# Optimization experiments

Measured on AMD Instinct MI355X. Metric: run time of the kernel, lower is better.

The kernel has to match this reference:

```python
import jax, jax.numpy as jnp
import numpy as np

D_MODEL = 1024
NUM_HEADS = 16
THETA = 10000.0


def _rope(x, pos):
    # x: [B, H, S, d_k], pos: [B, S] int
    d = x.shape[-1]
    half = d // 2
    inv_freq = THETA ** (-(jnp.arange(half, dtype=jnp.float32) * 2.0) / d)  # [half]
    ang = pos.astype(jnp.float32)[..., None] * inv_freq                     # [B, S, half]
    cos = jnp.cos(ang)[:, None, :, :]  # [B, 1, S, half]
    sin = jnp.sin(ang)[:, None, :, :]
    x1 = x[..., 0::2]
    x2 = x[..., 1::2]
    r1 = x1 * cos - x2 * sin
    r2 = x1 * sin + x2 * cos
    return jnp.stack([r1, r2], axis=-1).reshape(x.shape)


def setup_inputs() -> dict:
    key = jax.random.key(0)
    ks = jax.random.split(key, 5)
    B, S, D = 2, 2048, D_MODEL
    scale = 1.0 / np.sqrt(D)
    x = jax.random.normal(ks[0], (B, S, D), dtype=jnp.float32)
    token_positions = jnp.broadcast_to(jnp.arange(S, dtype=jnp.int32), (B, S))
    Wq = jax.random.normal(ks[1], (D, D), dtype=jnp.float32) * scale
    Wk = jax.random.normal(ks[2], (D, D), dtype=jnp.float32) * scale
    Wv = jax.random.normal(ks[3], (D, D), dtype=jnp.float32) * scale
    Wo = jax.random.normal(ks[4], (D, D), dtype=jnp.float32) * scale
    return {"x": x, "token_positions": token_positions, "Wq": Wq, "Wk": Wk, "Wv": Wv, "Wo": Wo}


def reference(x, token_positions, Wq, Wk, Wv, Wo):
    B, S, D = x.shape
    H = NUM_HEADS
    dk = D // H
    # Linear: y = x @ W.T (torch nn.Linear convention, no bias)
    q = jnp.einsum('bsd,od->bso', x, Wq).reshape(B, S, H, dk).transpose(0, 2, 1, 3)
    k = jnp.einsum('bsd,od->bso', x, Wk).reshape(B, S, H, dk).transpose(0, 2, 1, 3)
    v = jnp.einsum('bsd,od->bso', x, Wv).reshape(B, S, H, dk).transpose(0, 2, 1, 3)
    q = _rope(q, token_positions)
    k = _rope(k, token_positions)
    scores = jnp.einsum('bhqd,bhkd->bhqk', q, k) / jnp.sqrt(jnp.float32(dk))
    causal = jnp.tril(jnp.ones((S, S), dtype=bool))
    scores = jnp.where(causal, scores, jnp.finfo(scores.dtype).min)
    attn = jax.nn.softmax(scores, axis=-1)
    out = jnp.einsum('bhqk,bhkd->bhqd', attn, v)  # [B, H, S, dk]
    out = out.transpose(0, 2, 1, 3).reshape(B, S, D)
    return jnp.einsum('bsd,od->bso', out, Wo)
```

## Files before the change

### kernel.cpp

```cpp
#include <hip/hip_runtime.h>
#include <stdint.h>

#define S_LEN 2048
#define DMODEL 1024
#define NHEAD 16
#define DK 64
#define BATCH 2

typedef __attribute__((ext_vector_type(8))) short bf16x8;
typedef __attribute__((ext_vector_type(4))) float f32x4;
typedef __attribute__((ext_vector_type(16))) float f32x16;
typedef __attribute__((ext_vector_type(2))) unsigned int uint2v;

__device__ __forceinline__ unsigned short f2bf(float f) {
  union { float f; unsigned u; } x; x.f = f;
  unsigned u = x.u;
  return (unsigned short)((u + 0x7fffu + ((u >> 16) & 1u)) >> 16);
}

__device__ __forceinline__ uint cvt_pk_bf16(float a, float b) {
  uint r;
  asm("v_cvt_pk_bf16_f32 %0, %1, %2" : "=v"(r) : "v"(a), "v"(b));
  return r;
}

__device__ __forceinline__ uint2v permswap(uint a, uint b) {
#if __has_builtin(__builtin_amdgcn_permlane32_swap)
  auto rr = __builtin_amdgcn_permlane32_swap(a, b, false, false);
  uint2v r; r.x = rr[0]; r.y = rr[1];
  return r;
#else
  uint ax = __shfl_xor(a, 32), bx = __shfl_xor(b, 32);
  int hi = (threadIdx.x & 63) >> 5;
  uint2v r; r.x = hi ? bx : a; r.y = hi ? b : ax;
  return r;
#endif
}

__device__ __forceinline__ void gload_lds16(const void* g, void* l) {
  __builtin_amdgcn_global_load_lds(
      (const __attribute__((address_space(1))) unsigned int*)g,
      (__attribute__((address_space(3))) unsigned int*)l, 16, 0, 0);
}

#define QSCALE 0.18033688011112042f

__global__ __launch_bounds__(256) void cast_inputs(
    const float4* __restrict__ x,
    const float4* __restrict__ wq, const float4* __restrict__ wk,
    const float4* __restrict__ wv, const float4* __restrict__ wo,
    ushort4* __restrict__ xb, ushort4* __restrict__ wqkvb, ushort4* __restrict__ wob,
    const int* __restrict__ pos, float2* __restrict__ rope)
{
  int i = blockIdx.x * 256 + threadIdx.x;
  const int NCAST = (1 << 21);
  if (i < NCAST) {
    float4 v; ushort4* dst;
    if (i < (1 << 20)) {
      v = x[i]; dst = xb + i;
    } else {
      int j = i - (1 << 20);
      int wsel = j >> 18;
      int o = j & ((1 << 18) - 1);
      const float4* src = (wsel == 0) ? wq : (wsel == 1) ? wk : (wsel == 2) ? wv : wo;
      v = src[o];
      dst = (wsel < 3) ? (wqkvb + ((size_t)wsel << 18) + o) : (wob + o);
    }
    ushort4 r;
    r.x = f2bf(v.x); r.y = f2bf(v.y); r.z = f2bf(v.z); r.w = f2bf(v.w);
    *dst = r;
  } else {
    int idx = i - NCAST;
    if (idx < 4096 * 32) {
      int ps = idx >> 5;
      int fi = idx & 31;
      float p = (float)pos[ps];
      float freq = exp2f(-(float)fi * 0.41524101186092096f);
      float ang = p * freq;
      rope[idx] = make_float2(cosf(ang), sinf(ang));
    }
  }
}

template<int EPI>
__global__ __launch_bounds__(256) void gemm_bt(
    const ushort* __restrict__ A, const ushort* __restrict__ Bw,
    const float2* __restrict__ rope,
    ushort* __restrict__ Qb, ushort* __restrict__ Kb, ushort* __restrict__ Vg,
    float* __restrict__ Out)
{
  constexpr int Kdim = 1024;
  __shared__ ushort At[128 * 64];
  __shared__ ushort Bt[128 * 64];
  const int bm = blockIdx.x & 31;
  const int bn = blockIdx.x >> 5;
  const int tid = threadIdx.x;
  const int w = tid >> 6, lane = tid & 63;
  const int wr = w >> 1, wc = w & 1;
  const int lrow = lane >> 3;
  const int lch = lane & 7;

  f32x4 acc[4][4];
#pragma unroll
  for (int i = 0; i < 4; ++i)
#pragma unroll
    for (int j = 0; j < 4; ++j) acc[i][j] = (f32x4){0.f, 0.f, 0.f, 0.f};

  const size_t abase = (size_t)(bm * 128) * Kdim;
  const size_t bbase = (size_t)(bn * 128) * Kdim;

  for (int kt = 0; kt < Kdim / 64; ++kt) {
#pragma unroll
    for (int inst = 0; inst < 4; ++inst) {
      int r = w * 32 + inst * 8 + lrow;
      int gc = lch ^ (r & 7);
      gload_lds16(A + abase + (size_t)r * Kdim + kt * 64 + gc * 8,
                  &At[(w * 32 + inst * 8) * 64]);
      gload_lds16(Bw + bbase + (size_t)r * Kdim + kt * 64 + gc * 8,
                  &Bt[(w * 32 + inst * 8) * 64]);
    }
    __syncthreads();
    __builtin_amdgcn_s_setprio(1);
#pragma unroll
    for (int kk = 0; kk < 2; ++kk) {
      bf16x8 af[4], bfv[4];
      int ch = kk * 4 + (lane >> 4);
#pragma unroll
      for (int fm = 0; fm < 4; ++fm) {
        int row = wr * 64 + fm * 16 + (lane & 15);
        af[fm] = *(const bf16x8*)&At[row * 64 + ((ch ^ (row & 7)) << 3)];
      }
#pragma unroll
      for (int fn = 0; fn < 4; ++fn) {
        int row = wc * 64 + fn * 16 + (lane & 15);
        bfv[fn] = *(const bf16x8*)&Bt[row * 64 + ((ch ^ (row & 7)) << 3)];
      }
#pragma unroll
      for (int fm = 0; fm < 4; ++fm)
#pragma unroll
        for (int fn = 0; fn < 4; ++fn)
          acc[fm][fn] = __builtin_amdgcn_mfma_f32_16x16x32_bf16(
              af[fm], bfv[fn], acc[fm][fn], 0, 0, 0);
    }
    __builtin_amdgcn_s_setprio(0);
    __syncthreads();
  }

  if constexpr (EPI == 0) {
    const int sel = bn >> 3;
    if (sel == 2) {
#pragma unroll
      for (int fn = 0; fn < 4; ++fn) {
        int gn = bn * 128 + wc * 64 + fn * 16 + (lane & 15);
        int col = gn & 1023;
        int h = col >> 6, d = col & 63;
#pragma unroll
        for (int fm = 0; fm < 4; ++fm) {
          int gm0 = bm * 128 + wr * 64 + fm * 16 + ((lane >> 4) << 2);
          int b = gm0 >> 11, s0 = gm0 & 2047;
          uint lo = (uint)f2bf(acc[fm][fn][0]) | ((uint)f2bf(acc[fm][fn][1]) << 16);
          uint hi2 = (uint)f2bf(acc[fm][fn][2]) | ((uint)f2bf(acc[fm][fn][3]) << 16);
          uint2 val; val.x = lo; val.y = hi2;
          *(uint2*)(Vg + ((size_t)((b * NHEAD + h) * DK + d) * S_LEN) + s0) = val;
        }
      }
    } else {
      ushort* dst0 = (sel == 0) ? Qb : Kb;
#pragma unroll
      for (int fn = 0; fn < 4; ++fn) {
        int gn = bn * 128 + wc * 64 + fn * 16 + (lane & 15);
        int col = gn & 1023;
        int h = col >> 6, d = col & 63;
#pragma unroll
        for (int fm = 0; fm < 4; ++fm) {
          int gm0 = bm * 128 + wr * 64 + fm * 16 + ((lane >> 4) << 2);
#pragma unroll
          for (int j = 0; j < 4; ++j) {
            int gm = gm0 + j;
            float v = acc[fm][fn][j];
            float p = __shfl_xor(v, 1);
            float2 cs = rope[gm * 32 + (d >> 1)];
            float r = (d & 1) ? (v * cs.x + p * cs.y) : (v * cs.x - p * cs.y);
            if (sel == 0) r *= QSCALE;
            int b = gm >> 11, s = gm & 2047;
            dst0[((size_t)(b * NHEAD + h) * S_LEN + s) * DK + d] = f2bf(r);
          }
        }
      }
    }
  } else {
#pragma unroll
    for (int fn = 0; fn < 4; ++fn) {
      int gn = bn * 128 + wc * 64 + fn * 16 + (lane & 15);
#pragma unroll
      for (int fm = 0; fm < 4; ++fm) {
        int gm0 = bm * 128 + wr * 64 + fm * 16 + ((lane >> 4) << 2);
#pragma unroll
        for (int j = 0; j < 4; ++j)
          Out[(size_t)(gm0 + j) * 1024 + gn] = acc[fm][fn][j];
      }
    }
  }
}

__global__ __launch_bounds__(256) void attn_kernel(
    const ushort* __restrict__ Qb, const ushort* __restrict__ Kb,
    const ushort* __restrict__ Vg, ushort* __restrict__ Ob)
{
  __shared__ ushort Kt[2][64 * 64];
  __shared__ ushort Vt[2][64 * 64];
  const int tid = threadIdx.x;
  const int w = tid >> 6, lane = tid & 63;
  const int hi = lane >> 5, q = lane & 31;
  const int ww = w & 1;
  const int bid = blockIdx.x;
  const int swz = (bid & 7) * 64 + (bid >> 3);
  const int bh = swz >> 4, pair = swz & 15;
  const size_t kqbase = (size_t)bh * (S_LEN * DK);
  const size_t vbase  = (size_t)bh * (DK * S_LEN);
  const int b = bh >> 4, h = bh & 15;
  const int qtw = (w < 2) ? (31 - pair) : pair;
  const int ktmax = 31 - pair;
  const int q0w = qtw * 64 + ww * 32;

  bf16x8 qf[4];
  {
    const ushort* qp = Qb + kqbase + (size_t)(q0w + q) * DK + hi * 8;
#pragma unroll
    for (int kk = 0; kk < 4; ++kk) qf[kk] = *(const bf16x8*)(qp + kk * 16);
  }
  f32x16 oacc[2];
#pragma unroll
  for (int dt = 0; dt < 2; ++dt)
#pragma unroll
    for (int r = 0; r < 16; ++r) oacc[dt][r] = 0.f;
  float m_r = -INFINITY, l_r = 0.f;

  const int srow = lane >> 3, sslot = lane & 7;

#define STAGE(buf_, kt_)                                                     \
  do {                                                                       \
    _Pragma("unroll") for (int p = 0; p < 2; ++p) {                          \
      int rr = p * 32 + w * 8 + srow;                                        \
      int gc = sslot ^ (rr & 7);                                             \
      gload_lds16(Kb + kqbase + (size_t)((kt_) * 64 + rr) * DK + gc * 8,     \
                  &Kt[buf_][(p * 32 + w * 8) * 64]);                         \
      gload_lds16(Vg + vbase + (size_t)rr * S_LEN + (kt_) * 64 + gc * 8,     \
                  &Vt[buf_][(p * 32 + w * 8) * 64]);                         \
    }                                                                        \
  } while (0)

  STAGE(0, 0);
  STAGE(1, 1);
  for (int kt = 0; kt <= ktmax; ++kt) {
    const int cur = kt & 1;
    if (kt < ktmax) asm volatile("s_waitcnt vmcnt(4)" ::: "memory");
    else            asm volatile("s_waitcnt vmcnt(0)" ::: "memory");
    __builtin_amdgcn_s_barrier();
    __builtin_amdgcn_sched_barrier(0);

    if (kt <= qtw) {
      const int nct = (kt == qtw && ww == 0) ? 1 : 2;
      f32x16 sacc[2];
#pragma unroll
      for (int ct = 0; ct < 2; ++ct)
#pragma unroll
        for (int r = 0; r < 16; ++r) sacc[ct][r] = 0.f;

      __builtin_amdgcn_s_setprio(1);
#pragma unroll
      for (int ct = 0; ct < 2; ++ct) {
        if (ct < nct) {
#pragma unroll
          for (int kk = 0; kk < 4; ++kk) {
            int row = ct * 32 + q;
            bf16x8 kf = *(const bf16x8*)
                &Kt[cur][row * 64 + (((kk * 2 + hi) ^ (row & 7)) << 3)];
            sacc[ct] = __builtin_amdgcn_mfma_f32_32x32x16_bf16(
                kf, qf[kk], sacc[ct], 0, 0, 0);
          }
        }
      }
      __builtin_amdgcn_s_setprio(0);

      if (kt == qtw) {
#pragma unroll
        for (int r = 0; r < 16; ++r) {
          int crow = (r & 3) + 8 * (r >> 2) + 4 * hi;
          bool m = crow > q;
          if (ww == 0) { if (m) sacc[0][r] = -INFINITY; }
          else         { if (m) sacc[1][r] = -INFINITY; }
        }
      }

      float mx = -INFINITY;
#pragma unroll
      for (int ct = 0; ct < 2; ++ct)
        if (ct < nct)
#pragma unroll
          for (int r = 0; r < 16; ++r) mx = fmaxf(mx, sacc[ct][r]);
      mx = fmaxf(mx, __shfl_xor(mx, 32));
      if (mx > m_r + 8.0f) {
        float sc = exp2f(m_r - mx);
        m_r = mx;
        l_r *= sc;
#pragma unroll
        for (int dt = 0; dt < 2; ++dt)
#pragma unroll
          for (int r = 0; r < 16; ++r) oacc[dt][r] *= sc;
      }
      float rs = 0.f;
#pragma unroll
      for (int ct = 0; ct < 2; ++ct)
        if (ct < nct)
#pragma unroll
          for (int r = 0; r < 16; ++r) {
            float e = exp2f(sacc[ct][r] - m_r);
            sacc[ct][r] = e;
            rs += e;
          }
      rs += __shfl_xor(rs, 32);
      l_r += rs;

#pragma unroll
      for (int ct = 0; ct < 2; ++ct) {
        if (ct < nct) {
          uint W8[8];
#pragma unroll
          for (int r4 = 0; r4 < 4; ++r4)
#pragma unroll
            for (int i = 0; i < 2; ++i)
              W8[r4 * 2 + i] = cvt_pk_bf16(sacc[ct][4 * r4 + 2 * i],
                                           sacc[ct][4 * r4 + 2 * i + 1]);
          __builtin_amdgcn_s_setprio(1);
#pragma unroll
          for (int kcl = 0; kcl < 2; ++kcl) {
            uint2v p0 = permswap(W8[4 * kcl],     W8[4 * kcl + 2]);
            uint2v p1 = permswap(W8[4 * kcl + 1], W8[4 * kcl + 3]);
            union { uint u[4]; bf16x8 v; } pb;
            pb.u[0] = p0.x; pb.u[1] = p1.x; pb.u[2] = p0.y; pb.u[3] = p1.y;
            int kc2 = ct * 2 + kcl;
#pragma unroll
            for (int dt = 0; dt < 2; ++dt) {
              int row = dt * 32 + q;
              bf16x8 vf = *(const bf16x8*)
                  &Vt[cur][row * 64 + (((kc2 * 2 + hi) ^ (row & 7)) << 3)];
              oacc[dt] = __builtin_amdgcn_mfma_f32_32x32x16_bf16(
                  vf, pb.v, oacc[dt], 0, 0, 0);
            }
          }
          __builtin_amdgcn_s_setprio(0);
        }
      }
    }

    __builtin_amdgcn_s_barrier();
    if (kt + 2 <= ktmax) STAGE(cur, kt + 2);
  }

  float inv = 1.0f / l_r;
  uint* Ow = (uint*)&Kt[0][0] + w * 1024;
#pragma unroll
  for (int dt = 0; dt < 2; ++dt)
#pragma unroll
    for (int r4 = 0; r4 < 4; ++r4)
#pragma unroll
      for (int i = 0; i < 2; ++i) {
        int wi = dt * 16 + r4 * 4 + hi * 2 + i;
        uint val = cvt_pk_bf16(oacc[dt][4 * r4 + 2 * i] * inv,
                               oacc[dt][4 * r4 + 2 * i + 1] * inv);
        Ow[q * 32 + (((wi >> 2) ^ (q & 7)) << 2) + (wi & 3)] = val;
      }
#pragma unroll
  for (int p = 0; p < 4; ++p) {
    int idx = p * 64 + lane;
    int qr = idx >> 3, c = idx & 7;
    bf16x8 v = *(const bf16x8*)
        &((const ushort*)Ow)[qr * 64 + ((c ^ (qr & 7)) << 3)];
    int gq = q0w + qr;
    *(bf16x8*)(Ob + ((size_t)b * S_LEN + gq) * DMODEL + h * DK + c * 8) = v;
  }
#undef STAGE
}

extern "C" void kernel_launch(void* const* d_in, const int* in_sizes, int n_in,
                              void* d_out, int out_size, void* d_ws, size_t ws_size,
                              hipStream_t stream) {
  const float* x  = (const float*)d_in[0];
  const int* pos  = (const int*)d_in[1];
  const float* wq = (const float*)d_in[2];
  const float* wk = (const float*)d_in[3];
  const float* wv = (const float*)d_in[4];
  const float* wo = (const float*)d_in[5];
  float* out = (float*)d_out;

  char* ws = (char*)d_ws;
  ushort* xb    = (ushort*)(ws);
  ushort* wqkvb = (ushort*)(ws + (size_t)( 8u << 20));
  ushort* wob   = (ushort*)(ws + (size_t)(14u << 20));
  float2* rope  = (float2*)(ws + (size_t)(16u << 20));
  ushort* Qb    = (ushort*)(ws + (size_t)(17u << 20));
  ushort* Kb    = (ushort*)(ws + (size_t)(25u << 20));
  ushort* Vg    = (ushort*)(ws + (size_t)(33u << 20));
  ushort* Ob    = (ushort*)(ws + (size_t)(41u << 20));

  cast_inputs<<<8704, 256, 0, stream>>>((const float4*)x, (const float4*)wq,
      (const float4*)wk, (const float4*)wv, (const float4*)wo,
      (ushort4*)xb, (ushort4*)wqkvb, (ushort4*)wob, pos, rope);
  gemm_bt<0><<<32 * 24, 256, 0, stream>>>(xb, wqkvb, rope, Qb, Kb, Vg, nullptr);
  attn_kernel<<<512, 256, 0, stream>>>(Qb, Kb, Vg, Ob);
  gemm_bt<1><<<32 * 8, 256, 0, stream>>>(Ob, wob, rope, nullptr, nullptr, nullptr, out);
}
```

Baseline: 148.0 us.

## Split attention KV range across wave pairs with direct global loads and merge

Restructures the attention kernel so that each block handles one 64-row query tile, and the two wave pairs split the key tiles by parity. The partial softmax states are then merged through shared memory. K and V fragments are now read straight from global memory into registers, which removes the LDS double-buffered staging and the per-iteration barriers. The grid doubles to 1024 blocks with launch_bounds(256,2) to raise occupancy and drop the paired causal-tile load balancing. The cost is uncoalesced, unshared global reads, since each wave loads its own K/V with no LDS reuse, plus an extra merge step.

```diff
diff --git a/kernel.cpp b/kernel.cpp
--- a/kernel.cpp
+++ b/kernel.cpp
@@ -203,25 +203,24 @@
   }
 }
 
-__global__ __launch_bounds__(256) void attn_kernel(
+__global__ __launch_bounds__(256, 2) void attn_kernel(
     const ushort* __restrict__ Qb, const ushort* __restrict__ Kb,
     const ushort* __restrict__ Vg, ushort* __restrict__ Ob)
 {
-  __shared__ ushort Kt[2][64 * 64];
-  __shared__ ushort Vt[2][64 * 64];
+  __shared__ float xbuf[2][64][34];
+  __shared__ ushort oscratch[2][2048];
   const int tid = threadIdx.x;
   const int w = tid >> 6, lane = tid & 63;
   const int hi = lane >> 5, q = lane & 31;
-  const int ww = w & 1;
+  const int rowhalf = w & 1, par = w >> 1;
   const int bid = blockIdx.x;
-  const int swz = (bid & 7) * 64 + (bid >> 3);
-  const int bh = swz >> 4, pair = swz & 15;
+  const int xcd = bid & 7, idx = bid >> 3;
+  const int bh = xcd * 4 + (idx >> 5);
+  const int qt = 31 - (idx & 31);
   const size_t kqbase = (size_t)bh * (S_LEN * DK);
   const size_t vbase  = (size_t)bh * (DK * S_LEN);
   const int b = bh >> 4, h = bh & 15;
-  const int qtw = (w < 2) ? (31 - pair) : pair;
-  const int ktmax = 31 - pair;
-  const int q0w = qtw * 64 + ww * 32;
+  const int q0w = qt * 64 + rowhalf * 32;
 
   bf16x8 qf[4];
   {
@@ -236,151 +235,152 @@
     for (int r = 0; r < 16; ++r) oacc[dt][r] = 0.f;
   float m_r = -INFINITY, l_r = 0.f;
 
-  const int srow = lane >> 3, sslot = lane & 7;
-
-#define STAGE(buf_, kt_)                                                     \
-  do {                                                                       \
-    _Pragma("unroll") for (int p = 0; p < 2; ++p) {                          \
-      int rr = p * 32 + w * 8 + srow;                                        \
-      int gc = sslot ^ (rr & 7);                                             \
-      gload_lds16(Kb + kqbase + (size_t)((kt_) * 64 + rr) * DK + gc * 8,     \
-                  &Kt[buf_][(p * 32 + w * 8) * 64]);                         \
-      gload_lds16(Vg + vbase + (size_t)rr * S_LEN + (kt_) * 64 + gc * 8,     \
-                  &Vt[buf_][(p * 32 + w * 8) * 64]);                         \
-    }                                                                        \
-  } while (0)
-
-  STAGE(0, 0);
-  STAGE(1, 1);
-  for (int kt = 0; kt <= ktmax; ++kt) {
-    const int cur = kt & 1;
-    if (kt < ktmax) asm volatile("s_waitcnt vmcnt(4)" ::: "memory");
-    else            asm volatile("s_waitcnt vmcnt(0)" ::: "memory");
-    __builtin_amdgcn_s_barrier();
-    __builtin_amdgcn_sched_barrier(0);
-
-    if (kt <= qtw) {
-      const int nct = (kt == qtw && ww == 0) ? 1 : 2;
-      f32x16 sacc[2];
-#pragma unroll
-      for (int ct = 0; ct < 2; ++ct)
-#pragma unroll
-        for (int r = 0; r < 16; ++r) sacc[ct][r] = 0.f;
-
-      __builtin_amdgcn_s_setprio(1);
-#pragma unroll
-      for (int ct = 0; ct < 2; ++ct) {
-        if (ct < nct) {
-#pragma unroll
-          for (int kk = 0; kk < 4; ++kk) {
-            int row = ct * 32 + q;
-            bf16x8 kf = *(const bf16x8*)
-                &Kt[cur][row * 64 + (((kk * 2 + hi) ^ (row & 7)) << 3)];
-            sacc[ct] = __builtin_amdgcn_mfma_f32_32x32x16_bf16(
-                kf, qf[kk], sacc[ct], 0, 0, 0);
-          }
+  for (int kt = par; kt <= qt; kt += 2) {
+    const ushort* kb = Kb + kqbase + (size_t)(kt * 64) * DK;
+    const ushort* vb = Vg + vbase + kt * 64;
+
+    bf16x8 kfr[8];
+#pragma unroll
+    for (int ct = 0; ct < 2; ++ct)
+#pragma unroll
+      for (int kk = 0; kk < 4; ++kk)
+        kfr[ct * 4 + kk] =
+            *(const bf16x8*)(kb + (ct * 32 + q) * DK + (kk * 2 + hi) * 8);
+
+    f32x16 sacc[2];
+#pragma unroll
+    for (int ct = 0; ct < 2; ++ct)
+#pragma unroll
+      for (int r = 0; r < 16; ++r) sacc[ct][r] = 0.f;
+
+    __builtin_amdgcn_s_setprio(1);
+#pragma unroll
+    for (int ct = 0; ct < 2; ++ct)
+#pragma unroll
+      for (int kk = 0; kk < 4; ++kk)
+        sacc[ct] = __builtin_amdgcn_mfma_f32_32x32x16_bf16(
+            kfr[ct * 4 + kk], qf[kk], sacc[ct], 0, 0, 0);
+    __builtin_amdgcn_s_setprio(0);
+
+    bf16x8 vfr[8];
+#pragma unroll
+    for (int kc2 = 0; kc2 < 4; ++kc2)
+#pragma unroll
+      for (int dt = 0; dt < 2; ++dt)
+        vfr[kc2 * 2 + dt] = *(const bf16x8*)
+            (vb + (dt * 32 + q) * S_LEN + (kc2 * 2 + hi) * 8);
+
+    if (kt == qt) {
+#pragma unroll
+      for (int r = 0; r < 16; ++r) {
+        int crow = (r & 3) + 8 * (r >> 2) + 4 * hi;
+        if (rowhalf == 0) {
+          if (crow > q) sacc[0][r] = -INFINITY;
+          sacc[1][r] = -INFINITY;
+        } else {
+          if (crow > q) sacc[1][r] = -INFINITY;
         }
       }
-      __builtin_amdgcn_s_setprio(0);
-
-      if (kt == qtw) {
-#pragma unroll
-        for (int r = 0; r < 16; ++r) {
-          int crow = (r & 3) + 8 * (r >> 2) + 4 * hi;
-          bool m = crow > q;
-          if (ww == 0) { if (m) sacc[0][r] = -INFINITY; }
-          else         { if (m) sacc[1][r] = -INFINITY; }
+    }
+
+    float mx = -INFINITY;
+#pragma unroll
+    for (int ct = 0; ct < 2; ++ct)
+#pragma unroll
+      for (int r = 0; r < 16; ++r) mx = fmaxf(mx, sacc[ct][r]);
+    mx = fmaxf(mx, __shfl_xor(mx, 32));
+    if (mx > m_r + 8.0f) {
+      float sc = exp2f(m_r - mx);
+      m_r = mx;
+      l_r *= sc;
+#pragma unroll
+      for (int dt = 0; dt < 2; ++dt)
+#pragma unroll
+        for (int r = 0; r < 16; ++r) oacc[dt][r] *= sc;
+    }
+    float rs = 0.f;
+#pragma unroll
+    for (int ct = 0; ct < 2; ++ct)
+#pragma unroll
+      for (int r = 0; r < 16; ++r) {
+        float e = exp2f(sacc[ct][r] - m_r);
+        sacc[ct][r] = e;
+        rs += e;
+      }
+    rs += __shfl_xor(rs, 32);
+    l_r += rs;
+
+    __builtin_amdgcn_s_setprio(1);
+#pragma unroll
+    for (int ct = 0; ct < 2; ++ct) {
+      uint W8[8];
+#pragma unroll
+      for (int r4 = 0; r4 < 4; ++r4)
+#pragma unroll
+        for (int i = 0; i < 2; ++i)
+          W8[r4 * 2 + i] = cvt_pk_bf16(sacc[ct][4 * r4 + 2 * i],
+                                       sacc[ct][4 * r4 + 2 * i + 1]);
+#pragma unroll
+      for (int kcl = 0; kcl < 2; ++kcl) {
+        uint2v p0 = permswap(W8[4 * kcl],     W8[4 * kcl + 2]);
+        uint2v p1 = permswap(W8[4 * kcl + 1], W8[4 * kcl + 3]);
+        union { uint u[4]; bf16x8 v; } pb;
+        pb.u[0] = p0.x; pb.u[1] = p1.x; pb.u[2] = p0.y; pb.u[3] = p1.y;
+        int kc2 = ct * 2 + kcl;
+#pragma unroll
+        for (int dt = 0; dt < 2; ++dt)
+          oacc[dt] = __builtin_amdgcn_mfma_f32_32x32x16_bf16(
+              vfr[kc2 * 2 + dt], pb.v, oacc[dt], 0, 0, 0);
+      }
+    }
+    __builtin_amdgcn_s_setprio(0);
+  }
+
+  if (par == 1) {
+#pragma unroll
+    for (int dt = 0; dt < 2; ++dt)
+#pragma unroll
+      for (int r = 0; r < 16; ++r) xbuf[rowhalf][lane][dt * 16 + r] = oacc[dt][r];
+    xbuf[rowhalf][lane][32] = m_r;
+    xbuf[rowhalf][lane][33] = l_r;
+  }
+  __syncthreads();
+  if (par == 0) {
+    float mB = xbuf[rowhalf][lane][32];
+    float lB = xbuf[rowhalf][lane][33];
+    float m2 = fmaxf(m_r, mB);
+    float sA = exp2f(m_r - m2);
+    float sB = exp2f(mB - m2);
+    l_r = l_r * sA + lB * sB;
+#pragma unroll
+    for (int dt = 0; dt < 2; ++dt)
+#pragma unroll
+      for (int r = 0; r < 16; ++r)
+        oacc[dt][r] = oacc[dt][r] * sA + xbuf[rowhalf][lane][dt * 16 + r] * sB;
+
+    float inv = 1.0f / l_r;
+    uint* Ow = (uint*)&oscratch[rowhalf][0];
+#pragma unroll
+    for (int dt = 0; dt < 2; ++dt)
+#pragma unroll
+      for (int r4 = 0; r4 < 4; ++r4)
+#pragma unroll
+        for (int i = 0; i < 2; ++i) {
+          int wi = dt * 16 + r4 * 4 + hi * 2 + i;
+          uint val = cvt_pk_bf16(oacc[dt][4 * r4 + 2 * i] * inv,
+                                 oacc[dt][4 * r4 + 2 * i + 1] * inv);
+          Ow[q * 32 + (((wi >> 2) ^ (q & 7)) << 2) + (wi & 3)] = val;
         }
-      }
-
-      float mx = -INFINITY;
-#pragma unroll
-      for (int ct = 0; ct < 2; ++ct)
-        if (ct < nct)
-#pragma unroll
-          for (int r = 0; r < 16; ++r) mx = fmaxf(mx, sacc[ct][r]);
-      mx = fmaxf(mx, __shfl_xor(mx, 32));
-      if (mx > m_r + 8.0f) {
-        float sc = exp2f(m_r - mx);
-        m_r = mx;
-        l_r *= sc;
-#pragma unroll
-        for (int dt = 0; dt < 2; ++dt)
-#pragma unroll
-          for (int r = 0; r < 16; ++r) oacc[dt][r] *= sc;
-      }
-      float rs = 0.f;
-#pragma unroll
-      for (int ct = 0; ct < 2; ++ct)
-        if (ct < nct)
-#pragma unroll
-          for (int r = 0; r < 16; ++r) {
-            float e = exp2f(sacc[ct][r] - m_r);
-            sacc[ct][r] = e;
-            rs += e;
-          }
-      rs += __shfl_xor(rs, 32);
-      l_r += rs;
-
-#pragma unroll
-      for (int ct = 0; ct < 2; ++ct) {
-        if (ct < nct) {
-          uint W8[8];
-#pragma unroll
-          for (int r4 = 0; r4 < 4; ++r4)
-#pragma unroll
-            for (int i = 0; i < 2; ++i)
-              W8[r4 * 2 + i] = cvt_pk_bf16(sacc[ct][4 * r4 + 2 * i],
-                                           sacc[ct][4 * r4 + 2 * i + 1]);
-          __builtin_amdgcn_s_setprio(1);
-#pragma unroll
-          for (int kcl = 0; kcl < 2; ++kcl) {
-            uint2v p0 = permswap(W8[4 * kcl],     W8[4 * kcl + 2]);
-            uint2v p1 = permswap(W8[4 * kcl + 1], W8[4 * kcl + 3]);
-            union { uint u[4]; bf16x8 v; } pb;
-            pb.u[0] = p0.x; pb.u[1] = p1.x; pb.u[2] = p0.y; pb.u[3] = p1.y;
-            int kc2 = ct * 2 + kcl;
-#pragma unroll
-            for (int dt = 0; dt < 2; ++dt) {
-              int row = dt * 32 + q;
-              bf16x8 vf = *(const bf16x8*)
-                  &Vt[cur][row * 64 + (((kc2 * 2 + hi) ^ (row & 7)) << 3)];
-              oacc[dt] = __builtin_amdgcn_mfma_f32_32x32x16_bf16(
-                  vf, pb.v, oacc[dt], 0, 0, 0);
-            }
-          }
-          __builtin_amdgcn_s_setprio(0);
-        }
-      }
-    }
-
-    __builtin_amdgcn_s_barrier();
-    if (kt + 2 <= ktmax) STAGE(cur, kt + 2);
-  }
-
-  float inv = 1.0f / l_r;
-  uint* Ow = (uint*)&Kt[0][0] + w * 1024;
-#pragma unroll
-  for (int dt = 0; dt < 2; ++dt)
-#pragma unroll
-    for (int r4 = 0; r4 < 4; ++r4)
-#pragma unroll
-      for (int i = 0; i < 2; ++i) {
-        int wi = dt * 16 + r4 * 4 + hi * 2 + i;
-        uint val = cvt_pk_bf16(oacc[dt][4 * r4 + 2 * i] * inv,
-                               oacc[dt][4 * r4 + 2 * i + 1] * inv);
-        Ow[q * 32 + (((wi >> 2) ^ (q & 7)) << 2) + (wi & 3)] = val;
-      }
-#pragma unroll
-  for (int p = 0; p < 4; ++p) {
-    int idx = p * 64 + lane;
-    int qr = idx >> 3, c = idx & 7;
-    bf16x8 v = *(const bf16x8*)
-        &((const ushort*)Ow)[qr * 64 + ((c ^ (qr & 7)) << 3)];
-    int gq = q0w + qr;
-    *(bf16x8*)(Ob + ((size_t)b * S_LEN + gq) * DMODEL + h * DK + c * 8) = v;
-  }
-#undef STAGE
+#pragma unroll
+    for (int p = 0; p < 4; ++p) {
+      int idx2 = p * 64 + lane;
+      int qr = idx2 >> 3, c = idx2 & 7;
+      bf16x8 v = *(const bf16x8*)
+          &((const ushort*)Ow)[qr * 64 + ((c ^ (qr & 7)) << 3)];
+      int gq = q0w + qr;
+      *(bf16x8*)(Ob + ((size_t)b * S_LEN + gq) * DMODEL + h * DK + c * 8) = v;
+    }
+  }
 }
 
 extern "C" void kernel_launch(void* const* d_in, const int* in_sizes, int n_in,
@@ -408,6 +408,6 @@
       (const float4*)wk, (const float4*)wv, (const float4*)wo,
       (ushort4*)xb, (ushort4*)wqkvb, (ushort4*)wob, pos, rope);
   gemm_bt<0><<<32 * 24, 256, 0, stream>>>(xb, wqkvb, rope, Qb, Kb, Vg, nullptr);
-  attn_kernel<<<512, 256, 0, stream>>>(Qb, Kb, Vg, Ob);
+  attn_kernel<<<1024, 256, 0, stream>>>(Qb, Kb, Vg, Ob);
   gemm_bt<1><<<32 * 8, 256, 0, stream>>>(Ob, wob, rope, nullptr, nullptr, nullptr, out);
 }
```

Measured after the change: 167.9 us. 1.13x slower.
